# Optimization experiments

Measured on AMD Instinct MI355X. Metric: run time of the kernel, lower is better.

Reference implementation:

```python
import jax, jax.numpy as jnp
import numpy as np
import math

BATCH, L, H, P = 8, 2048, 1024, 512
DT_MIN, DT_MAX = 1e-3, 1e-1
STEP_RESCALE = 1.0


def setup_inputs() -> dict:
    key = jax.random.key(0)
    ks = jax.random.split(key, 8)
    signal = jax.random.normal(ks[0], (BATCH, L, H), dtype=jnp.float32)
    prev_state = jnp.zeros((BATCH, P), dtype=jnp.float32)
    # S5-style init: Lambda_re < 0, Lambda_im = pi * k
    Lambda_re = -0.5 * jnp.ones((P,), dtype=jnp.float32)
    Lambda_im = math.pi * jnp.arange(P, dtype=jnp.float32)
    # B stored as real (P,H,2) -> complex B_tilde; lecun scale 1/sqrt(H)
    B = jax.random.normal(ks[1], (P, H, 2), dtype=jnp.float32) / math.sqrt(H)
    # C stored as real (H,P,2) -> complex C_tilde; lecun scale 1/sqrt(P)
    C = jax.random.normal(ks[2], (H, P, 2), dtype=jnp.float32) / math.sqrt(P)
    D = jax.random.normal(ks[3], (H,), dtype=jnp.float32)
    u = jax.random.uniform(ks[4], (P, 1), dtype=jnp.float32)
    log_step = u * (math.log(DT_MAX) - math.log(DT_MIN)) + math.log(DT_MIN)
    return {"signal": signal, "prev_state": prev_state,
            "Lambda_re": Lambda_re, "Lambda_im": Lambda_im,
            "B": B, "C": C, "D": D, "log_step": log_step}


def _binop(qi, qj):
    # parallel-scan combine for diagonal linear recurrence x_t = A_t x_{t-1} + b_t
    A_i, b_i = qi
    A_j, b_j = qj
    return (A_j * A_i, b_j + A_j * b_i)


def reference(signal, prev_state, Lambda_re, Lambda_im, B, C, D, log_step):
    Lambda = Lambda_re + 1j * Lambda_im                      # (P,) complex
    B_tilde = B[..., 0] + 1j * B[..., 1]                     # (P,H)
    C_tilde = C[..., 0] + 1j * C[..., 1]                     # (H,P)
    step = STEP_RESCALE * jnp.exp(log_step[:, 0])            # (P,)
    # zero-order hold discretization
    Lambda_bar = jnp.exp(Lambda * step)                      # (P,)
    B_bar = ((Lambda_bar - 1.0) / Lambda)[:, None] * B_tilde # (P,H)
    # Bu elements: (BATCH, L, P) complex
    Bu = jnp.einsum('blh,ph->blp', signal.astype(B_bar.dtype), B_bar)
    # A elements: Lambda_bar tiled over time; first element carries prev_state
    A_first = (Lambda_bar[None, :] * prev_state.astype(Lambda_bar.dtype))[:, None, :]
    A_rest = jnp.broadcast_to(Lambda_bar, (signal.shape[0], signal.shape[1] - 1, Lambda_bar.shape[0]))
    A = jnp.concatenate([A_first, A_rest], axis=1)           # (BATCH, L, P)
    _, xs = jax.lax.associative_scan(_binop, (A, Bu), axis=1)  # xs: (BATCH, L, P)
    # conj_sym=True -> 2 * Re(C_tilde @ x), plus feedthrough D*u
    y = 2.0 * jnp.einsum('blp,hp->blh', xs, C_tilde).real + D * signal
    state = xs[:, -1]                                        # (BATCH, P) complex
    return y, state
```

## Files before the change

kernel.cpp:

```cpp
#include <hip/hip_runtime.h>
#include <math.h>

#define L_SEQ   2048
#define BATCH_N 8
#define H_DIM   1024
#define P_DIM   512
#define M_DIM   (BATCH_N * L_SEQ)
#define N2      1024
#define NC      32
#define T_CHUNK 64

typedef __attribute__((ext_vector_type(8))) __bf16 bf16x8;
typedef __attribute__((ext_vector_type(4))) float f32x4;

__device__ __forceinline__ unsigned f2bf_bits(float f) {
    unsigned u = __builtin_bit_cast(unsigned, f);
    return (u + 0x7fffu + ((u >> 16) & 1u)) >> 16;
}
__device__ __forceinline__ float bf_lo(unsigned v) {
    return __builtin_bit_cast(float, v << 16);
}
__device__ __forceinline__ float bf_hi(unsigned v) {
    return __builtin_bit_cast(float, v & 0xffff0000u);
}
__device__ __forceinline__ float bf2f(unsigned short u) {
    return __builtin_bit_cast(float, (unsigned)u << 16);
}

#define ASYNC_COPY16(gsrc, ldst)                                            \
    __builtin_amdgcn_global_load_lds(                                       \
        (__attribute__((address_space(1))) void*)(gsrc),                    \
        (__attribute__((address_space(3))) void*)(ldst), 16, 0, 0)

#define NB_CONV 16384
#define NB_W    4096

__global__ __launch_bounds__(256) void prep(
    const float* __restrict__ signal, unsigned short* __restrict__ sigbf,
    const float* __restrict__ Lre_in, const float* __restrict__ Lim_in,
    const float* __restrict__ log_step,
    const float* __restrict__ B, const float* __restrict__ C,
    unsigned short* __restrict__ W1, unsigned short* __restrict__ W2,
    float* __restrict__ lam)
{
    int bid = blockIdx.x;
    if (bid < NB_CONV) {
        size_t i = ((size_t)bid * 256 + threadIdx.x) * 4;
        float4 v = *(const float4*)(signal + i);
        ushort4 o;
        o.x = (unsigned short)f2bf_bits(v.x);
        o.y = (unsigned short)f2bf_bits(v.y);
        o.z = (unsigned short)f2bf_bits(v.z);
        o.w = (unsigned short)f2bf_bits(v.w);
        *(ushort4*)(sigbf + i) = o;
    } else if (bid < NB_CONV + NB_W) {
        int idx = (bid - NB_CONV) * 256 + threadIdx.x;
        if (idx < P_DIM * H_DIM) {
            int p = idx >> 10;
            int h = idx & (H_DIM - 1);
            float step = expf(log_step[p]);
            float c = Lre_in[p];
            float d = Lim_in[p];
            float mag = expf(c * step);
            float ang = d * step;
            float lr = mag * cosf(ang);
            float li = mag * sinf(ang);
            float a = lr - 1.0f, bb = li;
            float inv = 1.0f / (c * c + d * d);
            float gre = (a * c + bb * d) * inv;
            float gim = (bb * c - a * d) * inv;
            float bre = B[(size_t)idx * 2];
            float bim = B[(size_t)idx * 2 + 1];
            W1[(size_t)p * H_DIM + h]           = (unsigned short)f2bf_bits(gre * bre - gim * bim);
            W1[(size_t)(P_DIM + p) * H_DIM + h] = (unsigned short)f2bf_bits(gre * bim + gim * bre);
        } else {
            int j = idx - P_DIM * H_DIM;
            int h = j >> 9;
            int p = j & (P_DIM - 1);
            float cre = C[(size_t)j * 2];
            float cim = C[(size_t)j * 2 + 1];
            W2[(size_t)h * N2 + p]         = (unsigned short)f2bf_bits( 2.0f * cre);
            W2[(size_t)h * N2 + P_DIM + p] = (unsigned short)f2bf_bits(-2.0f * cim);
        }
    } else {
        int p = (bid - (NB_CONV + NB_W)) * 256 + threadIdx.x;
        if (p < P_DIM) {
            float step = expf(log_step[p]);
            float c = Lre_in[p];
            float d = Lim_in[p];
            float mag = expf(c * step);
            float ang = d * step;
            lam[p]         = mag * cosf(ang);
            lam[P_DIM + p] = mag * sinf(ang);
        }
    }
}

template <int MODE>
__global__ __launch_bounds__(256, 4) void gemm_mfma(
    const unsigned short* __restrict__ A,
    const unsigned short* __restrict__ W,
    void* __restrict__ Out, int K,
    const float* __restrict__ Dvec, const unsigned short* __restrict__ SigBf)
{
    __shared__ unsigned short smem[128 * 64 * 2];
    unsigned short* As = smem;
    unsigned short* Ws = smem + 128 * 64;

    const int tid  = threadIdx.x;
    const int lane = tid & 63;
    const int wid  = tid >> 6;
    const int wm   = wid >> 1;
    const int wn   = wid & 1;

    const int id  = blockIdx.x;
    const int xcd = id & 7;
    const int j   = id >> 3;
    const int mb  = xcd * 16 + (j >> 3);
    const int nb  = j & 7;
    const int m0 = mb * 128;
    const int n0 = nb * 128;

    const int srow = tid >> 3;
    const int qg   = ((tid & 7) - ((tid >> 4) & 7)) & 7;
    const unsigned short* Abase = A + (size_t)(m0 + srow) * K + qg * 8;
    const unsigned short* Wbase = W + (size_t)(n0 + srow) * K + qg * 8;

    const int fr = lane & 15;
    const int fq = (lane >> 4) & 3;
    const int sw = fr >> 1;

    f32x4 acc[4][4] = {};

    for (int k0 = 0; k0 < K; k0 += 64) {
        __syncthreads();
        #pragma unroll
        for (int i = 0; i < 4; ++i)
            ASYNC_COPY16(Abase + (size_t)(i * 32) * K + k0,
                         As + (size_t)(i * 256 + wid * 64) * 8);
        #pragma unroll
        for (int i = 0; i < 4; ++i)
            ASYNC_COPY16(Wbase + (size_t)(i * 32) * K + k0,
                         Ws + (size_t)(i * 256 + wid * 64) * 8);
        __syncthreads();

        #pragma unroll
        for (int kk = 0; kk < 2; ++kk) {
            bf16x8 af[4], wf[4];
            #pragma unroll
            for (int mi = 0; mi < 4; ++mi) {
                int row = wm * 64 + mi * 16 + fr;
                int sl  = (kk * 4 + fq + sw) & 7;
                af[mi] = *(const bf16x8*)&As[(size_t)row * 64 + sl * 8];
            }
            #pragma unroll
            for (int ni = 0; ni < 4; ++ni) {
                int row = wn * 64 + ni * 16 + fr;
                int sl  = (kk * 4 + fq + sw) & 7;
                wf[ni] = *(const bf16x8*)&Ws[(size_t)row * 64 + sl * 8];
            }
            #pragma unroll
            for (int mi = 0; mi < 4; ++mi)
                #pragma unroll
                for (int ni = 0; ni < 4; ++ni)
                    acc[mi][ni] = __builtin_amdgcn_mfma_f32_16x16x32_bf16(
                        af[mi], wf[ni], acc[mi][ni], 0, 0, 0);
        }
    }

    if (MODE == 0) {
        unsigned short* T = smem;
        #pragma unroll
        for (int h = 0; h < 2; ++h) {
            __syncthreads();
            if (wm == h) {
                #pragma unroll
                for (int mi = 0; mi < 4; ++mi)
                    #pragma unroll
                    for (int ni = 0; ni < 4; ++ni)
                        #pragma unroll
                        for (int r = 0; r < 4; ++r) {
                            int lrow = mi * 16 + fq * 4 + r;
                            int lcol = wn * 64 + ni * 16 + fr;
                            T[lrow * 128 + lcol] =
                                (unsigned short)f2bf_bits(acc[mi][ni][r]);
                        }
            }
            __syncthreads();
            #pragma unroll
            for (int jj = 0; jj < 4; ++jj) {
                int chunk = jj * 256 + tid;
                int row = chunk >> 4;
                int co  = (chunk & 15) * 8;
                *(ulonglong2*)((unsigned short*)Out +
                    (size_t)(m0 + h * 64 + row) * 1024 + n0 + co) =
                    *(const ulonglong2*)&T[row * 128 + co];
            }
        }
    } else {
        float Dl[4];
        #pragma unroll
        for (int ni = 0; ni < 4; ++ni)
            Dl[ni] = Dvec[n0 + wn * 64 + ni * 16 + fr];
        #pragma unroll
        for (int mi = 0; mi < 4; ++mi) {
            #pragma unroll
            for (int ni = 0; ni < 4; ++ni) {
                #pragma unroll
                for (int r = 0; r < 4; ++r) {
                    int row = m0 + wm * 64 + mi * 16 + fq * 4 + r;
                    int col = n0 + wn * 64 + ni * 16 + fr;
                    float v = acc[mi][ni][r];
                    v = fmaf(Dl[ni], bf2f(SigBf[(size_t)row * 1024 + col]), v);
                    ((float*)Out)[(size_t)row * 1024 + col] = v;
                }
            }
        }
    }
}

__global__ __launch_bounds__(256) void scan_sums(
    const unsigned short* __restrict__ Bu, const float* __restrict__ lam,
    float* __restrict__ S)
{
    int b = blockIdx.x, c = blockIdx.y, t = threadIdx.x;
    int p0 = 2 * t, p1 = 2 * t + 1;
    float lr0 = lam[p0], li0 = lam[P_DIM + p0];
    float lr1 = lam[p1], li1 = lam[P_DIM + p1];
    const unsigned* base =
        (const unsigned*)(Bu + ((size_t)b * L_SEQ + (size_t)c * T_CHUNK) * N2);
    float xr0 = 0, xi0 = 0, xr1 = 0, xi1 = 0;
    for (int j0 = 0; j0 < T_CHUNK; j0 += 8) {
        unsigned R[8], I[8];
        #pragma unroll
        for (int j = 0; j < 8; ++j) {
            R[j] = base[(size_t)(j0 + j) * 512 + t];
            I[j] = base[(size_t)(j0 + j) * 512 + 256 + t];
        }
        #pragma unroll
        for (int j = 0; j < 8; ++j) {
            float nr0 = fmaf(lr0, xr0, fmaf(-li0, xi0, bf_lo(R[j])));
            float ni0 = fmaf(lr0, xi0, fmaf( li0, xr0, bf_lo(I[j])));
            float nr1 = fmaf(lr1, xr1, fmaf(-li1, xi1, bf_hi(R[j])));
            float ni1 = fmaf(lr1, xi1, fmaf( li1, xr1, bf_hi(I[j])));
            xr0 = nr0; xi0 = ni0; xr1 = nr1; xi1 = ni1;
        }
    }
    float* Sb = S + ((size_t)(b * NC + c) * 2) * P_DIM;
    Sb[p0] = xr0; Sb[p1] = xr1;
    Sb[P_DIM + p0] = xi0; Sb[P_DIM + p1] = xi1;
}

__global__ __launch_bounds__(256) void scan_apply(
    unsigned short* __restrict__ Bu, const float* __restrict__ lam,
    const float* __restrict__ S, float* __restrict__ out_state,
    int interleaved)
{
    int b = blockIdx.x, c = blockIdx.y, t = threadIdx.x;
    int p0 = 2 * t, p1 = 2 * t + 1;
    float lr0 = lam[p0], li0 = lam[P_DIM + p0];
    float lr1 = lam[p1], li1 = lam[P_DIM + p1];

    float pr0 = lr0, pi0 = li0, pr1 = lr1, pi1 = li1;
    #pragma unroll
    for (int i = 0; i < 6; ++i) {
        float a0 = pr0 * pr0 - pi0 * pi0, b0 = 2.0f * pr0 * pi0;
        float a1 = pr1 * pr1 - pi1 * pi1, b1 = 2.0f * pr1 * pi1;
        pr0 = a0; pi0 = b0; pr1 = a1; pi1 = b1;
    }

    float2 sre[NC - 1], sim[NC - 1];
    #pragma unroll
    for (int k = 0; k < NC - 1; ++k) {
        const float* Sb = S + ((size_t)(b * NC + k) * 2) * P_DIM;
        sre[k] = *(const float2*)&Sb[p0];
        sim[k] = *(const float2*)&Sb[P_DIM + p0];
    }

    float xr0 = 0, xi0 = 0, xr1 = 0, xi1 = 0;
    float cr0 = 0, ci0 = 0, cr1 = 0, ci1 = 0;
    #pragma unroll
    for (int k = 0; k < NC - 1; ++k) {
        if (k == c) { cr0 = xr0; ci0 = xi0; cr1 = xr1; ci1 = xi1; }
        float nr0 = fmaf(pr0, xr0, fmaf(-pi0, xi0, sre[k].x));
        float ni0 = fmaf(pr0, xi0, fmaf( pi0, xr0, sim[k].x));
        float nr1 = fmaf(pr1, xr1, fmaf(-pi1, xi1, sre[k].y));
        float ni1 = fmaf(pr1, xi1, fmaf( pi1, xr1, sim[k].y));
        xr0 = nr0; xi0 = ni0; xr1 = nr1; xi1 = ni1;
    }
    if (c == NC - 1) { cr0 = xr0; ci0 = xi0; cr1 = xr1; ci1 = xi1; }

    xr0 = cr0; xi0 = ci0; xr1 = cr1; xi1 = ci1;
    unsigned* base =
        (unsigned*)(Bu + ((size_t)b * L_SEQ + (size_t)c * T_CHUNK) * N2);
    for (int j0 = 0; j0 < T_CHUNK; j0 += 8) {
        unsigned R[8], I[8];
        #pragma unroll
        for (int j = 0; j < 8; ++j) {
            R[j] = base[(size_t)(j0 + j) * 512 + t];
            I[j] = base[(size_t)(j0 + j) * 512 + 256 + t];
        }
        #pragma unroll
        for (int j = 0; j < 8; ++j) {
            float nr0 = fmaf(lr0, xr0, fmaf(-li0, xi0, bf_lo(R[j])));
            float ni0 = fmaf(lr0, xi0, fmaf( li0, xr0, bf_lo(I[j])));
            float nr1 = fmaf(lr1, xr1, fmaf(-li1, xi1, bf_hi(R[j])));
            float ni1 = fmaf(lr1, xi1, fmaf( li1, xr1, bf_hi(I[j])));
            xr0 = nr0; xi0 = ni0; xr1 = nr1; xi1 = ni1;
            R[j] = f2bf_bits(nr0) | (f2bf_bits(nr1) << 16);
            I[j] = f2bf_bits(ni0) | (f2bf_bits(ni1) << 16);
        }
        #pragma unroll
        for (int j = 0; j < 8; ++j) {
            base[(size_t)(j0 + j) * 512 + t]       = R[j];
            base[(size_t)(j0 + j) * 512 + 256 + t] = I[j];
        }
    }
    if (c == NC - 1) {
        if (interleaved) {
            out_state[((size_t)b * P_DIM + p0) * 2]     = xr0;
            out_state[((size_t)b * P_DIM + p0) * 2 + 1] = xi0;
            out_state[((size_t)b * P_DIM + p1) * 2]     = xr1;
            out_state[((size_t)b * P_DIM + p1) * 2 + 1] = xi1;
        } else {
            out_state[(size_t)b * P_DIM + p0] = xr0;
            out_state[(size_t)b * P_DIM + p1] = xr1;
        }
    }
}

extern "C" void kernel_launch(void* const* d_in, const int* in_sizes, int n_in,
                              void* d_out, int out_size, void* d_ws, size_t ws_size,
                              hipStream_t stream)
{
    const float* signal   = (const float*)d_in[0];
    const float* Lre      = (const float*)d_in[2];
    const float* Lim      = (const float*)d_in[3];
    const float* B        = (const float*)d_in[4];
    const float* C        = (const float*)d_in[5];
    const float* Dv       = (const float*)d_in[6];
    const float* log_step = (const float*)d_in[7];

    char* ws = (char*)d_ws;
    unsigned short* sigbf = (unsigned short*)ws;
    unsigned short* Bubf  = (unsigned short*)(ws + 33554432);
    unsigned short* W1bf  = (unsigned short*)(ws + 67108864);
    unsigned short* W2bf  = (unsigned short*)(ws + 69206016);
    float*          lam   = (float*)(ws + 71303168);
    float*          S     = (float*)(ws + 71311360);
    size_t need = 71835648;
    if (ws_size < need) return;

    float* y_out = (float*)d_out;
    float* state_out = y_out + (size_t)M_DIM * H_DIM;
    int interleaved = (out_size - M_DIM * H_DIM) >= 2 * BATCH_N * P_DIM;

    prep<<<dim3(NB_CONV + NB_W + 2), dim3(256), 0, stream>>>(
        signal, sigbf, Lre, Lim, log_step, B, C, W1bf, W2bf, lam);

    gemm_mfma<0><<<dim3(1024), dim3(256), 0, stream>>>(
        sigbf, W1bf, Bubf, H_DIM, nullptr, nullptr);

    scan_sums<<<dim3(BATCH_N, NC), dim3(256), 0, stream>>>(Bubf, lam, S);
    scan_apply<<<dim3(BATCH_N, NC), dim3(256), 0, stream>>>(
        Bubf, lam, S, state_out, interleaved);

    gemm_mfma<1><<<dim3(1024), dim3(256), 0, stream>>>(
        Bubf, W2bf, y_out, N2, Dv, sigbf);
}
```

Measured before the change: 224.5 us.

## Fuse scan passes into one kernel with per-batch atomic grid barrier

Merges the chunk-sum and apply scan kernels into one launch. Blocks of the same batch publish their chunk sums, then wait on an atomic counter (reset in prep) until all chunks are done before applying the carries. This removes one kernel launch and gap, and the second pass may hit cached Bu data. It relies on all 256 blocks being co-resident to avoid deadlock, and spinning blocks occupy CUs while they wait.

Measured after the change: 259.7 us. +15.6%, slower.

```diff
diff --git a/kernel.cpp b/kernel.cpp
--- a/kernel.cpp
+++ b/kernel.cpp
@@ -41,7 +41,7 @@
     const float* __restrict__ log_step,
     const float* __restrict__ B, const float* __restrict__ C,
     unsigned short* __restrict__ W1, unsigned short* __restrict__ W2,
-    float* __restrict__ lam)
+    float* __restrict__ lam, int* __restrict__ cnt)
 {
     int bid = blockIdx.x;
     if (bid < NB_CONV) {
@@ -93,6 +93,8 @@
             lam[p]         = mag * cosf(ang);
             lam[P_DIM + p] = mag * sinf(ang);
         }
+        if (bid == NB_CONV + NB_W && threadIdx.x < BATCH_N)
+            cnt[threadIdx.x] = 0;
     }
 }
 
@@ -219,47 +221,52 @@
     }
 }
 
-__global__ __launch_bounds__(256) void scan_sums(
-    const unsigned short* __restrict__ Bu, const float* __restrict__ lam,
-    float* __restrict__ S)
+__global__ __launch_bounds__(256) void scan_fused(
+    unsigned short* __restrict__ Bu, const float* __restrict__ lam,
+    float* __restrict__ S, int* __restrict__ cnt,
+    float* __restrict__ out_state, int interleaved)
 {
     int b = blockIdx.x, c = blockIdx.y, t = threadIdx.x;
     int p0 = 2 * t, p1 = 2 * t + 1;
     float lr0 = lam[p0], li0 = lam[P_DIM + p0];
     float lr1 = lam[p1], li1 = lam[P_DIM + p1];
-    const unsigned* base =
-        (const unsigned*)(Bu + ((size_t)b * L_SEQ + (size_t)c * T_CHUNK) * N2);
-    float xr0 = 0, xi0 = 0, xr1 = 0, xi1 = 0;
-    for (int j0 = 0; j0 < T_CHUNK; j0 += 8) {
-        unsigned R[8], I[8];
-        #pragma unroll
-        for (int j = 0; j < 8; ++j) {
-            R[j] = base[(size_t)(j0 + j) * 512 + t];
-            I[j] = base[(size_t)(j0 + j) * 512 + 256 + t];
-        }
-        #pragma unroll
-        for (int j = 0; j < 8; ++j) {
-            float nr0 = fmaf(lr0, xr0, fmaf(-li0, xi0, bf_lo(R[j])));
-            float ni0 = fmaf(lr0, xi0, fmaf( li0, xr0, bf_lo(I[j])));
-            float nr1 = fmaf(lr1, xr1, fmaf(-li1, xi1, bf_hi(R[j])));
-            float ni1 = fmaf(lr1, xi1, fmaf( li1, xr1, bf_hi(I[j])));
-            xr0 = nr0; xi0 = ni0; xr1 = nr1; xi1 = ni1;
-        }
-    }
-    float* Sb = S + ((size_t)(b * NC + c) * 2) * P_DIM;
-    Sb[p0] = xr0; Sb[p1] = xr1;
-    Sb[P_DIM + p0] = xi0; Sb[P_DIM + p1] = xi1;
-}
-
-__global__ __launch_bounds__(256) void scan_apply(
-    unsigned short* __restrict__ Bu, const float* __restrict__ lam,
-    const float* __restrict__ S, float* __restrict__ out_state,
-    int interleaved)
-{
-    int b = blockIdx.x, c = blockIdx.y, t = threadIdx.x;
-    int p0 = 2 * t, p1 = 2 * t + 1;
-    float lr0 = lam[p0], li0 = lam[P_DIM + p0];
-    float lr1 = lam[p1], li1 = lam[P_DIM + p1];
+    unsigned* base =
+        (unsigned*)(Bu + ((size_t)b * L_SEQ + (size_t)c * T_CHUNK) * N2);
+
+    {
+        float xr0 = 0, xi0 = 0, xr1 = 0, xi1 = 0;
+        for (int j0 = 0; j0 < T_CHUNK; j0 += 8) {
+            unsigned R[8], I[8];
+            #pragma unroll
+            for (int j = 0; j < 8; ++j) {
+                R[j] = base[(size_t)(j0 + j) * 512 + t];
+                I[j] = base[(size_t)(j0 + j) * 512 + 256 + t];
+            }
+            #pragma unroll
+            for (int j = 0; j < 8; ++j) {
+                float nr0 = fmaf(lr0, xr0, fmaf(-li0, xi0, bf_lo(R[j])));
+                float ni0 = fmaf(lr0, xi0, fmaf( li0, xr0, bf_lo(I[j])));
+                float nr1 = fmaf(lr1, xr1, fmaf(-li1, xi1, bf_hi(R[j])));
+                float ni1 = fmaf(lr1, xi1, fmaf( li1, xr1, bf_hi(I[j])));
+                xr0 = nr0; xi0 = ni0; xr1 = nr1; xi1 = ni1;
+            }
+        }
+        float* Sb = S + ((size_t)(b * NC + c) * 2) * P_DIM;
+        Sb[p0] = xr0; Sb[p1] = xr1;
+        Sb[P_DIM + p0] = xi0; Sb[P_DIM + p1] = xi1;
+    }
+
+    __threadfence();
+    __syncthreads();
+    if (t == 0) {
+        __hip_atomic_fetch_add(&cnt[b], 1, __ATOMIC_ACQ_REL,
+                               __HIP_MEMORY_SCOPE_AGENT);
+        while (__hip_atomic_load(&cnt[b], __ATOMIC_ACQUIRE,
+                                 __HIP_MEMORY_SCOPE_AGENT) < NC)
+            __builtin_amdgcn_s_sleep(8);
+        __threadfence();
+    }
+    __syncthreads();
 
     float pr0 = lr0, pi0 = li0, pr1 = lr1, pi1 = li1;
     #pragma unroll
@@ -291,8 +298,6 @@
     if (c == NC - 1) { cr0 = xr0; ci0 = xi0; cr1 = xr1; ci1 = xi1; }
 
     xr0 = cr0; xi0 = ci0; xr1 = cr1; xi1 = ci1;
-    unsigned* base =
-        (unsigned*)(Bu + ((size_t)b * L_SEQ + (size_t)c * T_CHUNK) * N2);
     for (int j0 = 0; j0 < T_CHUNK; j0 += 8) {
         unsigned R[8], I[8];
         #pragma unroll
@@ -347,6 +352,7 @@
     unsigned short* W1bf  = (unsigned short*)(ws + 67108864);
     unsigned short* W2bf  = (unsigned short*)(ws + 69206016);
     float*          lam   = (float*)(ws + 71303168);
+    int*            cnt   = (int*)(ws + 71303168 + 4096);
     float*          S     = (float*)(ws + 71311360);
     size_t need = 71835648;
     if (ws_size < need) return;
@@ -356,14 +362,13 @@
     int interleaved = (out_size - M_DIM * H_DIM) >= 2 * BATCH_N * P_DIM;
 
     prep<<<dim3(NB_CONV + NB_W + 2), dim3(256), 0, stream>>>(
-        signal, sigbf, Lre, Lim, log_step, B, C, W1bf, W2bf, lam);
+        signal, sigbf, Lre, Lim, log_step, B, C, W1bf, W2bf, lam, cnt);
 
     gemm_mfma<0><<<dim3(1024), dim3(256), 0, stream>>>(
         sigbf, W1bf, Bubf, H_DIM, nullptr, nullptr);
 
-    scan_sums<<<dim3(BATCH_N, NC), dim3(256), 0, stream>>>(Bubf, lam, S);
-    scan_apply<<<dim3(BATCH_N, NC), dim3(256), 0, stream>>>(
-        Bubf, lam, S, state_out, interleaved);
+    scan_fused<<<dim3(BATCH_N, NC), dim3(256), 0, stream>>>(
+        Bubf, lam, S, cnt, state_out, interleaved);
 
     gemm_mfma<1><<<dim3(1024), dim3(256), 0, stream>>>(
         Bubf, W2bf, y_out, N2, Dv, sigbf);
```

## Split scan into more, smaller chunks with wider per-thread vectorized loads

Applied to the files above, without the earlier changes.

Doubles the number of time chunks from 32 to 64, halving each chunk's length, so the two scan kernels expose more parallel work. Each 256-thread block now covers two chunks, one chunk per pair of waves. Each thread handles four state channels using 64-bit Bu loads and 128-bit lambda and prefix loads, and holds a whole chunk in registers. The carry-in step in scan_apply becomes a Horner loop over earlier chunks only, with double-buffered loads of the partial sums, and the chunk-sum buffer S now reuses the W1 workspace region, which is no longer needed once the first GEMM has run. The cost is higher register pressure (launch_bounds with one block minimum) and correctness depends on W1 being dead at that point.

Result: no change. 225.9 us (+0.6%).

```diff
diff --git a/kernel.cpp b/kernel.cpp
--- a/kernel.cpp
+++ b/kernel.cpp
@@ -7,8 +7,8 @@
 #define P_DIM   512
 #define M_DIM   (BATCH_N * L_SEQ)
 #define N2      1024
-#define NC      32
-#define T_CHUNK 64
+#define NC      64
+#define T_CHUNK 32
 
 typedef __attribute__((ext_vector_type(8))) __bf16 bf16x8;
 typedef __attribute__((ext_vector_type(4))) float f32x4;
@@ -219,112 +219,163 @@
     }
 }
 
-__global__ __launch_bounds__(256) void scan_sums(
+__global__ __launch_bounds__(256, 1) void scan_sums(
     const unsigned short* __restrict__ Bu, const float* __restrict__ lam,
     float* __restrict__ S)
 {
-    int b = blockIdx.x, c = blockIdx.y, t = threadIdx.x;
-    int p0 = 2 * t, p1 = 2 * t + 1;
-    float lr0 = lam[p0], li0 = lam[P_DIM + p0];
-    float lr1 = lam[p1], li1 = lam[P_DIM + p1];
+    const int b = blockIdx.x, cg = blockIdx.y;
+    const int w = threadIdx.x >> 6, l = threadIdx.x & 63;
+    const int c    = cg * 2 + (w >> 1);
+    const int half = w & 1;
+    const int off  = half * 256 + 4 * l;
+    const int wo   = half * 128 + 2 * l;
+
+    float lr[4], li[4];
+    {
+        float4 t0 = *(const float4*)&lam[off];
+        float4 t1 = *(const float4*)&lam[P_DIM + off];
+        lr[0]=t0.x; lr[1]=t0.y; lr[2]=t0.z; lr[3]=t0.w;
+        li[0]=t1.x; li[1]=t1.y; li[2]=t1.z; li[3]=t1.w;
+    }
+
     const unsigned* base =
-        (const unsigned*)(Bu + ((size_t)b * L_SEQ + (size_t)c * T_CHUNK) * N2);
-    float xr0 = 0, xi0 = 0, xr1 = 0, xi1 = 0;
-    for (int j0 = 0; j0 < T_CHUNK; j0 += 8) {
-        unsigned R[8], I[8];
-        #pragma unroll
-        for (int j = 0; j < 8; ++j) {
-            R[j] = base[(size_t)(j0 + j) * 512 + t];
-            I[j] = base[(size_t)(j0 + j) * 512 + 256 + t];
-        }
-        #pragma unroll
-        for (int j = 0; j < 8; ++j) {
-            float nr0 = fmaf(lr0, xr0, fmaf(-li0, xi0, bf_lo(R[j])));
-            float ni0 = fmaf(lr0, xi0, fmaf( li0, xr0, bf_lo(I[j])));
-            float nr1 = fmaf(lr1, xr1, fmaf(-li1, xi1, bf_hi(R[j])));
-            float ni1 = fmaf(lr1, xi1, fmaf( li1, xr1, bf_hi(I[j])));
-            xr0 = nr0; xi0 = ni0; xr1 = nr1; xi1 = ni1;
+        (const unsigned*)Bu + ((size_t)b * L_SEQ + (size_t)c * T_CHUNK) * 512;
+
+    uint2 R[T_CHUNK], I[T_CHUNK];
+    #pragma unroll
+    for (int j = 0; j < T_CHUNK; ++j) {
+        R[j] = *(const uint2*)&base[(size_t)j * 512 + wo];
+        I[j] = *(const uint2*)&base[(size_t)j * 512 + 256 + wo];
+    }
+    float xr[4] = {}, xi[4] = {};
+    #pragma unroll
+    for (int j = 0; j < T_CHUNK; ++j) {
+        unsigned rw[2] = {R[j].x, R[j].y};
+        unsigned iw[2] = {I[j].x, I[j].y};
+        #pragma unroll
+        for (int k = 0; k < 2; ++k) {
+            int i0 = 2 * k, i1 = 2 * k + 1;
+            float nr0 = fmaf(lr[i0], xr[i0], fmaf(-li[i0], xi[i0], bf_lo(rw[k])));
+            float ni0 = fmaf(lr[i0], xi[i0], fmaf( li[i0], xr[i0], bf_lo(iw[k])));
+            float nr1 = fmaf(lr[i1], xr[i1], fmaf(-li[i1], xi[i1], bf_hi(rw[k])));
+            float ni1 = fmaf(lr[i1], xi[i1], fmaf( li[i1], xr[i1], bf_hi(iw[k])));
+            xr[i0]=nr0; xi[i0]=ni0; xr[i1]=nr1; xi[i1]=ni1;
         }
     }
     float* Sb = S + ((size_t)(b * NC + c) * 2) * P_DIM;
-    Sb[p0] = xr0; Sb[p1] = xr1;
-    Sb[P_DIM + p0] = xi0; Sb[P_DIM + p1] = xi1;
-}
-
-__global__ __launch_bounds__(256) void scan_apply(
+    *(float4*)&Sb[off]         = make_float4(xr[0], xr[1], xr[2], xr[3]);
+    *(float4*)&Sb[P_DIM + off] = make_float4(xi[0], xi[1], xi[2], xi[3]);
+}
+
+__global__ __launch_bounds__(256, 1) void scan_apply(
     unsigned short* __restrict__ Bu, const float* __restrict__ lam,
     const float* __restrict__ S, float* __restrict__ out_state,
     int interleaved)
 {
-    int b = blockIdx.x, c = blockIdx.y, t = threadIdx.x;
-    int p0 = 2 * t, p1 = 2 * t + 1;
-    float lr0 = lam[p0], li0 = lam[P_DIM + p0];
-    float lr1 = lam[p1], li1 = lam[P_DIM + p1];
-
-    float pr0 = lr0, pi0 = li0, pr1 = lr1, pi1 = li1;
-    #pragma unroll
-    for (int i = 0; i < 6; ++i) {
-        float a0 = pr0 * pr0 - pi0 * pi0, b0 = 2.0f * pr0 * pi0;
-        float a1 = pr1 * pr1 - pi1 * pi1, b1 = 2.0f * pr1 * pi1;
-        pr0 = a0; pi0 = b0; pr1 = a1; pi1 = b1;
-    }
-
-    float2 sre[NC - 1], sim[NC - 1];
-    #pragma unroll
-    for (int k = 0; k < NC - 1; ++k) {
-        const float* Sb = S + ((size_t)(b * NC + k) * 2) * P_DIM;
-        sre[k] = *(const float2*)&Sb[p0];
-        sim[k] = *(const float2*)&Sb[P_DIM + p0];
-    }
-
-    float xr0 = 0, xi0 = 0, xr1 = 0, xi1 = 0;
-    float cr0 = 0, ci0 = 0, cr1 = 0, ci1 = 0;
-    #pragma unroll
-    for (int k = 0; k < NC - 1; ++k) {
-        if (k == c) { cr0 = xr0; ci0 = xi0; cr1 = xr1; ci1 = xi1; }
-        float nr0 = fmaf(pr0, xr0, fmaf(-pi0, xi0, sre[k].x));
-        float ni0 = fmaf(pr0, xi0, fmaf( pi0, xr0, sim[k].x));
-        float nr1 = fmaf(pr1, xr1, fmaf(-pi1, xi1, sre[k].y));
-        float ni1 = fmaf(pr1, xi1, fmaf( pi1, xr1, sim[k].y));
-        xr0 = nr0; xi0 = ni0; xr1 = nr1; xi1 = ni1;
-    }
-    if (c == NC - 1) { cr0 = xr0; ci0 = xi0; cr1 = xr1; ci1 = xi1; }
-
-    xr0 = cr0; xi0 = ci0; xr1 = cr1; xi1 = ci1;
+    const int b = blockIdx.x, cg = blockIdx.y;
+    const int w = threadIdx.x >> 6, l = threadIdx.x & 63;
+    const int c    = cg * 2 + (w >> 1);
+    const int half = w & 1;
+    const int off  = half * 256 + 4 * l;
+    const int wo   = half * 128 + 2 * l;
+
+    float lr[4], li[4];
+    {
+        float4 t0 = *(const float4*)&lam[off];
+        float4 t1 = *(const float4*)&lam[P_DIM + off];
+        lr[0]=t0.x; lr[1]=t0.y; lr[2]=t0.z; lr[3]=t0.w;
+        li[0]=t1.x; li[1]=t1.y; li[2]=t1.z; li[3]=t1.w;
+    }
+
+    float pr[4], pi[4];
+    #pragma unroll
+    for (int i = 0; i < 4; ++i) { pr[i] = lr[i]; pi[i] = li[i]; }
+    #pragma unroll
+    for (int s = 0; s < 5; ++s)
+        #pragma unroll
+        for (int i = 0; i < 4; ++i) {
+            float a  = pr[i] * pr[i] - pi[i] * pi[i];
+            float bb = 2.0f * pr[i] * pi[i];
+            pr[i] = a; pi[i] = bb;
+        }
+
+    const float* Sbase = S + (size_t)b * NC * 2 * P_DIM + off;
+    float cr[4] = {}, ci[4] = {};
+    float bRA[8][4], bIA[8][4], bRB[8][4], bIB[8][4];
+
+#define LOADB(BR, BI, K0)                                                   \
+    _Pragma("unroll")                                                       \
+    for (int kk = 0; kk < 8; ++kk) {                                        \
+        float4 t0 = *(const float4*)&Sbase[(size_t)((K0) + kk) * 2 * P_DIM];\
+        float4 t1 = *(const float4*)&Sbase[(size_t)((K0) + kk) * 2 * P_DIM + P_DIM];\
+        BR[kk][0]=t0.x; BR[kk][1]=t0.y; BR[kk][2]=t0.z; BR[kk][3]=t0.w;     \
+        BI[kk][0]=t1.x; BI[kk][1]=t1.y; BI[kk][2]=t1.z; BI[kk][3]=t1.w;     \
+    }
+#define HORN(BR, BI, K0)                                                    \
+    _Pragma("unroll")                                                       \
+    for (int kk = 0; kk < 8; ++kk) {                                        \
+        if ((K0) + kk < c) {                                                \
+            _Pragma("unroll")                                               \
+            for (int i = 0; i < 4; ++i) {                                   \
+                float nr = fmaf(pr[i], cr[i], fmaf(-pi[i], ci[i], BR[kk][i]));\
+                float ni = fmaf(pr[i], ci[i], fmaf( pi[i], cr[i], BI[kk][i]));\
+                cr[i] = nr; ci[i] = ni;                                     \
+            }                                                               \
+        }                                                                   \
+    }
+
+    LOADB(bRA, bIA, 0)
+    #pragma unroll 1
+    for (int k0 = 0; k0 < NC; k0 += 16) {
+        LOADB(bRB, bIB, k0 + 8)
+        HORN(bRA, bIA, k0)
+        if (k0 + 16 < NC) { LOADB(bRA, bIA, k0 + 16) }
+        HORN(bRB, bIB, k0 + 8)
+    }
+#undef LOADB
+#undef HORN
+
     unsigned* base =
-        (unsigned*)(Bu + ((size_t)b * L_SEQ + (size_t)c * T_CHUNK) * N2);
-    for (int j0 = 0; j0 < T_CHUNK; j0 += 8) {
-        unsigned R[8], I[8];
-        #pragma unroll
-        for (int j = 0; j < 8; ++j) {
-            R[j] = base[(size_t)(j0 + j) * 512 + t];
-            I[j] = base[(size_t)(j0 + j) * 512 + 256 + t];
-        }
-        #pragma unroll
-        for (int j = 0; j < 8; ++j) {
-            float nr0 = fmaf(lr0, xr0, fmaf(-li0, xi0, bf_lo(R[j])));
-            float ni0 = fmaf(lr0, xi0, fmaf( li0, xr0, bf_lo(I[j])));
-            float nr1 = fmaf(lr1, xr1, fmaf(-li1, xi1, bf_hi(R[j])));
-            float ni1 = fmaf(lr1, xi1, fmaf( li1, xr1, bf_hi(I[j])));
-            xr0 = nr0; xi0 = ni0; xr1 = nr1; xi1 = ni1;
-            R[j] = f2bf_bits(nr0) | (f2bf_bits(nr1) << 16);
-            I[j] = f2bf_bits(ni0) | (f2bf_bits(ni1) << 16);
-        }
-        #pragma unroll
-        for (int j = 0; j < 8; ++j) {
-            base[(size_t)(j0 + j) * 512 + t]       = R[j];
-            base[(size_t)(j0 + j) * 512 + 256 + t] = I[j];
-        }
+        (unsigned*)Bu + ((size_t)b * L_SEQ + (size_t)c * T_CHUNK) * 512;
+    uint2 R[T_CHUNK], I[T_CHUNK];
+    #pragma unroll
+    for (int j = 0; j < T_CHUNK; ++j) {
+        R[j] = *(const uint2*)&base[(size_t)j * 512 + wo];
+        I[j] = *(const uint2*)&base[(size_t)j * 512 + 256 + wo];
+    }
+    float xr[4], xi[4];
+    #pragma unroll
+    for (int i = 0; i < 4; ++i) { xr[i] = cr[i]; xi[i] = ci[i]; }
+    #pragma unroll
+    for (int j = 0; j < T_CHUNK; ++j) {
+        unsigned rw[2] = {R[j].x, R[j].y};
+        unsigned iw[2] = {I[j].x, I[j].y};
+        #pragma unroll
+        for (int k = 0; k < 2; ++k) {
+            int i0 = 2 * k, i1 = 2 * k + 1;
+            float nr0 = fmaf(lr[i0], xr[i0], fmaf(-li[i0], xi[i0], bf_lo(rw[k])));
+            float ni0 = fmaf(lr[i0], xi[i0], fmaf( li[i0], xr[i0], bf_lo(iw[k])));
+            float nr1 = fmaf(lr[i1], xr[i1], fmaf(-li[i1], xi[i1], bf_hi(rw[k])));
+            float ni1 = fmaf(lr[i1], xi[i1], fmaf( li[i1], xr[i1], bf_hi(iw[k])));
+            xr[i0]=nr0; xi[i0]=ni0; xr[i1]=nr1; xi[i1]=ni1;
+            rw[k] = f2bf_bits(nr0) | (f2bf_bits(nr1) << 16);
+            iw[k] = f2bf_bits(ni0) | (f2bf_bits(ni1) << 16);
+        }
+        uint2 ro; ro.x = rw[0]; ro.y = rw[1];
+        uint2 io; io.x = iw[0]; io.y = iw[1];
+        *(uint2*)&base[(size_t)j * 512 + wo]       = ro;
+        *(uint2*)&base[(size_t)j * 512 + 256 + wo] = io;
     }
     if (c == NC - 1) {
-        if (interleaved) {
-            out_state[((size_t)b * P_DIM + p0) * 2]     = xr0;
-            out_state[((size_t)b * P_DIM + p0) * 2 + 1] = xi0;
-            out_state[((size_t)b * P_DIM + p1) * 2]     = xr1;
-            out_state[((size_t)b * P_DIM + p1) * 2 + 1] = xi1;
-        } else {
-            out_state[(size_t)b * P_DIM + p0] = xr0;
-            out_state[(size_t)b * P_DIM + p1] = xr1;
+        #pragma unroll
+        for (int i = 0; i < 4; ++i) {
+            int p = off + i;
+            if (interleaved) {
+                out_state[((size_t)b * P_DIM + p) * 2]     = xr[i];
+                out_state[((size_t)b * P_DIM + p) * 2 + 1] = xi[i];
+            } else {
+                out_state[(size_t)b * P_DIM + p] = xr[i];
+            }
         }
     }
 }
@@ -347,7 +398,7 @@
     unsigned short* W1bf  = (unsigned short*)(ws + 67108864);
     unsigned short* W2bf  = (unsigned short*)(ws + 69206016);
     float*          lam   = (float*)(ws + 71303168);
-    float*          S     = (float*)(ws + 71311360);
+    float*          S     = (float*)(ws + 67108864);
     size_t need = 71835648;
     if (ws_size < need) return;
 
@@ -361,8 +412,8 @@
     gemm_mfma<0><<<dim3(1024), dim3(256), 0, stream>>>(
         sigbf, W1bf, Bubf, H_DIM, nullptr, nullptr);
 
-    scan_sums<<<dim3(BATCH_N, NC), dim3(256), 0, stream>>>(Bubf, lam, S);
-    scan_apply<<<dim3(BATCH_N, NC), dim3(256), 0, stream>>>(
+    scan_sums<<<dim3(BATCH_N, NC / 2), dim3(256), 0, stream>>>(Bubf, lam, S);
+    scan_apply<<<dim3(BATCH_N, NC / 2), dim3(256), 0, stream>>>(
         Bubf, lam, S, state_out, interleaved);
 
     gemm_mfma<1><<<dim3(1024), dim3(256), 0, stream>>>(
```
